# Kernel optimization log

Hardware: AMD Instinct MI355X
Metric: run time of the kernel (lower is better)

Reference implementation:

```python
import jax, jax.numpy as jnp
import numpy as np

N_NODES = 100000
N_EDGES = 3200000
N_GRAPHS = 512
F_IN = 128
HID = 256
N_LABELS = 10


def setup_inputs() -> dict:
    key = jax.random.key(0)
    ks = jax.random.split(key, 16)
    x = jax.random.normal(ks[0], (N_NODES, F_IN), dtype=jnp.float32)
    edge_index = jax.random.randint(ks[1], (2, N_EDGES), 0, N_NODES)
    batch = jnp.sort(jax.random.randint(ks[2], (N_NODES,), 0, N_GRAPHS))
    dims = [(F_IN, HID), (HID, HID), (HID, HID), (HID, HID // 2), (HID // 2, HID // 2), (HID // 2, HID // 4)]
    inp = {"x": x, "edge_index": edge_index, "batch": batch, "primary_idxs_in_batch": 0}
    for i, (di, do) in enumerate(dims, 1):
        inp[f"W{i}"] = jax.random.normal(ks[2 + i], (di, do), dtype=jnp.float32) * (1.0 / np.sqrt(di))
        inp[f"b{i}"] = jnp.zeros((do,), dtype=jnp.float32)
    inp["Wlin"] = jax.random.normal(ks[12], (HID // 4, N_LABELS), dtype=jnp.float32) * (1.0 / np.sqrt(HID // 4))
    inp["blin"] = jnp.zeros((N_LABELS,), dtype=jnp.float32)
    return inp


def _gcn_conv(h, W, b, src, dst, norm):
    # dense transform first (smaller of the two sides), then normalized scatter-aggregate
    m = (h @ W)[src] * norm[:, None]  # [E+N, C_out]
    return jax.ops.segment_sum(m, dst, num_segments=N_NODES) + b


def reference(x, edge_index, batch, primary_idxs_in_batch,
              W1, b1, W2, b2, W3, b3, W4, b4, W5, b5, W6, b6, Wlin, blin):
    loops = jnp.arange(N_NODES, dtype=edge_index.dtype)
    src = jnp.concatenate([edge_index[0], loops])  # A + I (self loops)
    dst = jnp.concatenate([edge_index[1], loops])
    deg = jax.ops.segment_sum(jnp.ones_like(dst, dtype=x.dtype), dst, num_segments=N_NODES)
    dinv = jnp.where(deg > 0, jax.lax.rsqrt(deg), 0.0)
    norm = dinv[src] * dinv[dst]  # D^-1/2 (A+I) D^-1/2 edge weights

    h = jax.nn.relu(_gcn_conv(x, W1, b1, src, dst, norm))
    h = jax.nn.relu(_gcn_conv(h, W2, b2, src, dst, norm))
    h = jax.nn.relu(_gcn_conv(h, W3, b3, src, dst, norm))
    h = jax.nn.relu(_gcn_conv(h, W4, b4, src, dst, norm))
    h = jax.nn.relu(_gcn_conv(h, W5, b5, src, dst, norm))
    h = _gcn_conv(h, W6, b6, src, dst, norm)

    # primary_idxs_in_batch is falsy (0) -> global_mean_pool path
    s = jax.ops.segment_sum(h, batch, num_segments=N_GRAPHS)
    cnt = jax.ops.segment_sum(jnp.ones((N_NODES,), dtype=h.dtype), batch, num_segments=N_GRAPHS)
    pooled = s / jnp.maximum(cnt, 1.0)[:, None]  # [G, HID//4]

    logits = pooled @ Wlin + blin  # [G, labels]
    return (jax.nn.log_softmax(logits, axis=1), jax.nn.softmax(logits, axis=1))
```

## Files before the change

### kernel.cpp

```cpp
#include <hip/hip_runtime.h>
#include <math.h>

#define NN 100000
#define NE 3200000
#define NG 512
#define NBK 782
#define EBLK 782

typedef __attribute__((ext_vector_type(8))) short short8;
typedef __attribute__((ext_vector_type(4))) float f32x4;
typedef __attribute__((ext_vector_type(2))) float f32x2;

__device__ __forceinline__ float bf2f(unsigned short h){
  return __uint_as_float(((unsigned int)h) << 16);
}
__device__ __forceinline__ unsigned short f2bf(float f){
  unsigned int u = __float_as_uint(f);
  unsigned int r = (u + 0x7fffu + ((u >> 16) & 1u)) >> 16;
  return (unsigned short)r;
}
__device__ __forceinline__ void unpack16(uint4 v, float* f){
  f32x2 p;
  p = __builtin_amdgcn_cvt_pk_f32_fp8(v.x, 0); f[0]=p[0];  f[1]=p[1];
  p = __builtin_amdgcn_cvt_pk_f32_fp8(v.x, 1); f[2]=p[0];  f[3]=p[1];
  p = __builtin_amdgcn_cvt_pk_f32_fp8(v.y, 0); f[4]=p[0];  f[5]=p[1];
  p = __builtin_amdgcn_cvt_pk_f32_fp8(v.y, 1); f[6]=p[0];  f[7]=p[1];
  p = __builtin_amdgcn_cvt_pk_f32_fp8(v.z, 0); f[8]=p[0];  f[9]=p[1];
  p = __builtin_amdgcn_cvt_pk_f32_fp8(v.z, 1); f[10]=p[0]; f[11]=p[1];
  p = __builtin_amdgcn_cvt_pk_f32_fp8(v.w, 0); f[12]=p[0]; f[13]=p[1];
  p = __builtin_amdgcn_cvt_pk_f32_fp8(v.w, 1); f[14]=p[0]; f[15]=p[1];
}
__device__ __forceinline__ unsigned char f2fp8(float v){
  int p = __builtin_amdgcn_cvt_pk_fp8_f32(v, v, 0, 0);
  return (unsigned char)p;
}

__global__ __launch_bounds__(256) void hist2_k(const int* __restrict__ ei,
    int* __restrict__ cnt, int* __restrict__ btot){
  __shared__ int lh[NBK];
  int t = threadIdx.x, b = blockIdx.x;
  for (int i=t; i<NBK; i+=256) lh[i] = 0;
  __syncthreads();
  int base = b*4096;
  #pragma unroll
  for (int u=0; u<16; u++){
    int e = base + u*256 + t;
    if (e < NE) atomicAdd(&lh[ei[NE + e] >> 7], 1);
  }
  __syncthreads();
  for (int i=t; i<NBK; i+=256){
    int v = lh[i];
    cnt[b*NBK + i] = v;
    if (v) atomicAdd(&btot[i], v);
  }
}
__global__ void bscan2_k(const int* __restrict__ btot, int* __restrict__ bptr){
  __shared__ int sc[1024];
  int t = threadIdx.x;
  int v = (t < NBK) ? btot[t] : 0;
  sc[t] = v; __syncthreads();
  for (int off=1; off<1024; off<<=1){
    int u = (t>=off) ? sc[t-off] : 0;
    __syncthreads(); sc[t] += u; __syncthreads();
  }
  if (t < NBK) bptr[t] = sc[t] - v;
  if (t == 1023) bptr[NBK] = sc[1023];
}
__global__ __launch_bounds__(256) void bkpfx_k(int* __restrict__ cnt, const int* __restrict__ bptr){
  __shared__ int sc[256];
  int b = blockIdx.x, t = threadIdx.x;
  int carry = bptr[b];
  for (int base=0; base<EBLK; base+=256){
    int blk = base + t;
    int v = (blk < EBLK) ? cnt[blk*NBK + b] : 0;
    sc[t] = v; __syncthreads();
    for (int off=1; off<256; off<<=1){
      int u = (t>=off) ? sc[t-off] : 0;
      __syncthreads(); sc[t] += u; __syncthreads();
    }
    if (blk < EBLK) cnt[blk*NBK + b] = carry + sc[t] - v;
    carry += sc[255];
    __syncthreads();
  }
}
__global__ __launch_bounds__(256) void scat2_k(const int* __restrict__ ei,
    const int* __restrict__ cnt, uint2* __restrict__ ebuf){
  __shared__ int lh[NBK];
  __shared__ int lo[NBK];
  int t = threadIdx.x, b = blockIdx.x;
  for (int i=t; i<NBK; i+=256){ lh[i] = 0; lo[i] = cnt[b*NBK + i]; }
  __syncthreads();
  int base = b*4096;
  #pragma unroll
  for (int u=0; u<16; u++){
    int e = base + u*256 + t;
    if (e < NE){
      int s = ei[e], d = ei[NE + e];
      int bk = d >> 7;
      int r = atomicAdd(&lh[bk], 1);
      ebuf[lo[bk] + r] = make_uint2((unsigned)s, (unsigned)d);
    }
  }
}
__global__ __launch_bounds__(256) void bcsr_k(const uint2* __restrict__ ebuf,
    const int* __restrict__ bptr, int* __restrict__ rp, float* __restrict__ dinv,
    int* __restrict__ col){
  __shared__ int cnt[128];
  __shared__ int off[128];
  __shared__ int sc[128];
  int b = blockIdx.x, t = threadIdx.x;
  int nbase = b << 7;
  int beg = bptr[b], end = bptr[b+1];
  if (t < 128) cnt[t] = 0;
  __syncthreads();
  for (int e = beg + t; e < end; e += 256)
    atomicAdd(&cnt[(int)ebuf[e].y - nbase], 1);
  __syncthreads();
  int v = (t < 128) ? cnt[t] : 0;
  if (t < 128) sc[t] = v;
  __syncthreads();
  for (int o2=1; o2<128; o2<<=1){
    int u = (t < 128 && t >= o2) ? sc[t-o2] : 0;
    __syncthreads();
    if (t < 128) sc[t] += u;
    __syncthreads();
  }
  if (t < 128){
    int node = nbase + t;
    if (node < NN){
      int ex = beg + sc[t] - v;
      rp[node] = ex;
      off[t] = ex;
      dinv[node] = rsqrtf((float)(v + 1));
      cnt[t] = 0;
    }
  }
  if (b == ((NN-1) >> 7) && t == 0) rp[NN] = end;
  __syncthreads();
  for (int e = beg + t; e < end; e += 256){
    uint2 sd = ebuf[e];
    int li = (int)sd.y - nbase;
    int pos = off[li] + atomicAdd(&cnt[li], 1);
    col[pos] = (int)sd.x;
  }
}

__global__ void f2q_k(const float* __restrict__ in, unsigned char* __restrict__ out, int n4){
  int i = blockIdx.x*256 + threadIdx.x;
  if (i < n4){
    float4 v = ((const float4*)in)[i];
    int p = __builtin_amdgcn_cvt_pk_fp8_f32(v.x, v.y, 0, 0);
    p = __builtin_amdgcn_cvt_pk_fp8_f32(v.z, v.w, p, 1);
    ((unsigned int*)out)[i] = (unsigned int)p;
  }
}
__global__ void wswz_all_k(const float* W1, const float* W2, const float* W3,
                           const float* W4, const float* W5, const float* W6,
                           unsigned short* O1, unsigned short* O2, unsigned short* O3,
                           unsigned short* O4, unsigned short* O5, unsigned short* O6){
  int cfg = blockIdx.y;
  int K, N; const float* W; unsigned short* out;
  switch(cfg){
    case 0: K=128; N=256; W=W1; out=O1; break;
    case 1: K=256; N=256; W=W2; out=O2; break;
    case 2: K=256; N=256; W=W3; out=O3; break;
    case 3: K=256; N=128; W=W4; out=O4; break;
    case 4: K=128; N=128; W=W5; out=O5; break;
    default:K=128; N=64;  W=W6; out=O6; break;
  }
  int idx = blockIdx.x*256 + threadIdx.x;
  int total = K*N/8;
  if (idx >= total) return;
  int l = idx & 15;
  int t = idx >> 4; int q = t & 3; t >>= 2;
  int NT = N/16;
  int nt = t % NT, kt = t / NT;
  int kbase = kt*32 + q*8, n = nt*16 + l;
  short8 o;
  #pragma unroll
  for (int j=0;j<8;j++) o[j] = (short)f2bf(W[(size_t)(kbase+j)*N + n]);
  *(short8*)(out + (size_t)idx*8) = o;
}

template<int C, bool SRC_SCALE, bool RELU, bool HAS_BIAS>
__global__ __launch_bounds__(256) void spmm8_k(const unsigned char* __restrict__ in,
    unsigned short* __restrict__ out,
    const int* __restrict__ rp, const int* __restrict__ col,
    const float* __restrict__ dinv, const float* __restrict__ bias)
{
  constexpr int LPR = C/16;
  constexpr int RPW = 64/LPR;
  constexpr int RPB = 4*RPW;
  int tid = threadIdx.x;
  int wv = tid >> 6, lane = tid & 63;
  int sub = lane / LPR, li = lane % LPR;
  int row = blockIdx.x*RPB + wv*RPW + sub;
  if (row >= NN) return;
  int beg = rp[row], end = rp[row+1];
  float di = dinv[row];
  int co = li*16;
  const unsigned char* inb = in + co;
  float acc[16], tmp[16];
  unpack16(*(const uint4*)(inb + (size_t)row*C), acc);
  if (SRC_SCALE){
    #pragma unroll
    for (int v=0;v<16;v++) acc[v] *= di;
  }
  int j = beg;
  for (; j+8 <= end; j += 8){
    int s[8]; uint4 v[8]; float wgt[8];
    #pragma unroll
    for (int u=0;u<8;u++) s[u] = col[j+u];
    #pragma unroll
    for (int u=0;u<8;u++) v[u] = *(const uint4*)(inb + (size_t)s[u]*C);
    if (SRC_SCALE){
      #pragma unroll
      for (int u=0;u<8;u++) wgt[u] = dinv[s[u]];
    }
    #pragma unroll
    for (int u=0;u<8;u++){
      unpack16(v[u], tmp);
      float w = SRC_SCALE ? wgt[u] : 1.f;
      #pragma unroll
      for (int vv=0;vv<16;vv++) acc[vv] = fmaf(w, tmp[vv], acc[vv]);
    }
  }
  for (; j < end; j++){
    int ss = col[j];
    uint4 v = *(const uint4*)(inb + (size_t)ss*C);
    float w = SRC_SCALE ? dinv[ss] : 1.f;
    unpack16(v, tmp);
    #pragma unroll
    for (int vv=0;vv<16;vv++) acc[vv] = fmaf(w, tmp[vv], acc[vv]);
  }
  float bb[16];
  if (HAS_BIAS){
    #pragma unroll
    for (int u=0;u<4;u++) *(float4*)&bb[u*4] = *(const float4*)(bias + co + u*4);
  }
  #pragma unroll
  for (int v=0;v<16;v++){
    acc[v] *= di;
    if (HAS_BIAS) acc[v] += bb[v];
    if (RELU) acc[v] = fmaxf(acc[v], 0.f);
  }
  uint4 o0, o1;
  o0.x = (unsigned int)f2bf(acc[0])  | ((unsigned int)f2bf(acc[1])<<16);
  o0.y = (unsigned int)f2bf(acc[2])  | ((unsigned int)f2bf(acc[3])<<16);
  o0.z = (unsigned int)f2bf(acc[4])  | ((unsigned int)f2bf(acc[5])<<16);
  o0.w = (unsigned int)f2bf(acc[6])  | ((unsigned int)f2bf(acc[7])<<16);
  o1.x = (unsigned int)f2bf(acc[8])  | ((unsigned int)f2bf(acc[9])<<16);
  o1.y = (unsigned int)f2bf(acc[10]) | ((unsigned int)f2bf(acc[11])<<16);
  o1.z = (unsigned int)f2bf(acc[12]) | ((unsigned int)f2bf(acc[13])<<16);
  o1.w = (unsigned int)f2bf(acc[14]) | ((unsigned int)f2bf(acc[15])<<16);
  unsigned short* op = out + (size_t)row*C + co;
  *(uint4*)op = o0;
  *(uint4*)(op + 8) = o1;
}

template<int K, int N, int NB, int EPI>
__global__ __launch_bounds__(256) void mgemm_k(const unsigned short* __restrict__ A,
    const unsigned short* __restrict__ Bsw,
    const float* __restrict__ aux, unsigned short* __restrict__ Cb,
    unsigned char* __restrict__ Cq, int M)
{
  constexpr int NT = NB/16, KT = K/32;
  constexpr int KSTRIDE = (N/16)*64;
  __shared__ short8 Bl[2][NT*64];
  int tid = threadIdx.x;
  int w = tid >> 6, lane = tid & 63;
  int l = lane & 15, q = lane >> 4;
  int nb0 = blockIdx.y * NB;
  int rb = blockIdx.x*256 + w*64;
  const unsigned short* ap[4];
  #pragma unroll
  for (int rt=0; rt<4; rt++){
    int r = min(rb + rt*16 + l, M-1);
    ap[rt] = A + (size_t)r*K + q*8;
  }
  f32x4 acc[4][NT];
  #pragma unroll
  for (int rt=0; rt<4; rt++)
    #pragma unroll
    for (int nt=0; nt<NT; nt++) acc[rt][nt] = (f32x4){0,0,0,0};
  const short8* bsrc = (const short8*)Bsw + (size_t)(nb0/16)*64;
  for (int i=tid; i<NT*64; i+=256) Bl[0][i] = bsrc[i];
  short8 a[4], an[4];
  #pragma unroll
  for (int rt=0; rt<4; rt++) a[rt] = *(const short8*)(ap[rt]);
  for (int kt=0; kt<KT; kt++){
    __syncthreads();
    if (kt+1 < KT){
      const short8* s = bsrc + (size_t)(kt+1)*KSTRIDE;
      for (int i=tid; i<NT*64; i+=256) Bl[(kt+1)&1][i] = s[i];
      #pragma unroll
      for (int rt=0; rt<4; rt++) an[rt] = *(const short8*)(ap[rt] + (kt+1)*32);
    }
    const short8* bl = &Bl[kt&1][0];
    #pragma unroll
    for (int nt=0; nt<NT; nt++){
      short8 bf = bl[nt*64 + q*16 + l];
      acc[0][nt] = __builtin_amdgcn_mfma_f32_16x16x32_bf16(a[0], bf, acc[0][nt], 0,0,0);
      acc[1][nt] = __builtin_amdgcn_mfma_f32_16x16x32_bf16(a[1], bf, acc[1][nt], 0,0,0);
      acc[2][nt] = __builtin_amdgcn_mfma_f32_16x16x32_bf16(a[2], bf, acc[2][nt], 0,0,0);
      acc[3][nt] = __builtin_amdgcn_mfma_f32_16x16x32_bf16(a[3], bf, acc[3][nt], 0,0,0);
    }
    #pragma unroll
    for (int rt=0; rt<4; rt++) a[rt] = an[rt];
  }
  #pragma unroll
  for (int rt=0; rt<4; rt++){
    int rbb = rb + rt*16;
    #pragma unroll
    for (int nt=0; nt<NT; nt++){
      f32x4 av = acc[rt][nt];
      int n = nb0 + nt*16 + l;
      #pragma unroll
      for (int r=0;r<4;r++){
        int row = rbb + q*4 + r;
        if (row < M){
          float v = av[r];
          if (EPI == 0){
            v = fmaxf(v + aux[n], 0.f);
            Cb[(size_t)row*N + n] = f2bf(v);
          } else {
            v *= aux[row];
            Cq[(size_t)row*N + n] = f2fp8(v);
          }
        }
      }
    }
  }
}

__global__ __launch_bounds__(256) void poolhead_k(const unsigned short* __restrict__ h,
    const int* __restrict__ batch, const float* __restrict__ Wlin,
    const float* __restrict__ blin, float* __restrict__ out)
{
  __shared__ int range[2];
  __shared__ float red[4][64];
  __shared__ float pl[64];
  int g = blockIdx.x;
  if (threadIdx.x < 2){
    int target = g + threadIdx.x;
    int lo = 0, hi = NN;
    while (lo < hi){ int m = (lo+hi) >> 1; if (batch[m] < target) lo = m+1; else hi = m; }
    range[threadIdx.x] = lo;
  }
  __syncthreads();
  int lo = range[0], hi = range[1];
  int ch = threadIdx.x & 63, rg = threadIdx.x >> 6;
  float s = 0.f;
  for (int r = lo + rg; r < hi; r += 4) s += bf2f(h[(size_t)r*64 + ch]);
  red[rg][ch] = s; __syncthreads();
  if (rg == 0){
    float tot = red[0][ch] + red[1][ch] + red[2][ch] + red[3][ch];
    pl[ch] = tot / fmaxf((float)(hi - lo), 1.f);
  }
  __syncthreads();
  if (threadIdx.x == 0){
    float l[10];
    #pragma unroll
    for (int j=0;j<10;j++) l[j] = blin[j];
    for (int c=0;c<64;c++){
      float p = pl[c];
      #pragma unroll
      for (int j=0;j<10;j++) l[j] = fmaf(p, Wlin[c*10 + j], l[j]);
    }
    float mx = l[0];
    #pragma unroll
    for (int j=1;j<10;j++) mx = fmaxf(mx, l[j]);
    float e[10]; float se = 0.f;
    #pragma unroll
    for (int j=0;j<10;j++){ e[j] = expf(l[j]-mx); se += e[j]; }
    float lse = logf(se);
    #pragma unroll
    for (int j=0;j<10;j++){
      out[g*10 + j]         = l[j] - mx - lse;
      out[NG*10 + g*10 + j] = e[j] / se;
    }
  }
}

extern "C" void kernel_launch(void* const* d_in, const int* in_sizes, int n_in,
                              void* d_out, int out_size, void* d_ws, size_t ws_size,
                              hipStream_t stream)
{
  const float* x     = (const float*)d_in[0];
  const int*   ei    = (const int*)  d_in[1];
  const int*   batch = (const int*)  d_in[2];
  const float* W1=(const float*)d_in[4],  *b1=(const float*)d_in[5];
  const float* W2=(const float*)d_in[6],  *b2=(const float*)d_in[7];
  const float* W3=(const float*)d_in[8],  *b3=(const float*)d_in[9];
  const float* W4=(const float*)d_in[10], *b4=(const float*)d_in[11];
  const float* W5=(const float*)d_in[12], *b5=(const float*)d_in[13];
  const float* W6=(const float*)d_in[14], *b6=(const float*)d_in[15];
  const float* Wl=(const float*)d_in[16], *bl=(const float*)d_in[17];
  float* out = (float*)d_out;

  char* ws = (char*)d_ws;
  unsigned short* hA  = (unsigned short*)(ws + 0);
  unsigned short* hB  = (unsigned short*)(ws + 51200000);
  unsigned char*  hQ  = (unsigned char*) (ws + 102400000);
  unsigned char*  xq  = (unsigned char*) (ws + 128000000);
  int*   col   = (int*)  (ws + 140800000);
  uint2* ebuf  = (uint2*)(ws + 153600000);
  int*   rp    = (int*)  (ws + 179200000);
  float* dinv  = (float*)(ws + 180000016);
  unsigned short* W1s = (unsigned short*)(ws + 180400016);
  unsigned short* W2s = (unsigned short*)(ws + 180465552);
  unsigned short* W3s = (unsigned short*)(ws + 180596624);
  unsigned short* W4s = (unsigned short*)(ws + 180727696);
  unsigned short* W5s = (unsigned short*)(ws + 180793232);
  unsigned short* W6s = (unsigned short*)(ws + 180826000);
  int*   btot  = (int*)  (ws + 180842896);
  int*   bptr  = (int*)  (ws + 180846032);
  int*   cnt   = (int*)  (ws + 180849184);

  hipMemsetAsync(btot, 0, NBK*4, stream);

  hist2_k <<<EBLK, 256, 0, stream>>>(ei, cnt, btot);
  bscan2_k<<<1, 1024, 0, stream>>>(btot, bptr);
  bkpfx_k <<<NBK, 256, 0, stream>>>(cnt, bptr);
  scat2_k <<<EBLK, 256, 0, stream>>>(ei, cnt, ebuf);
  bcsr_k  <<<NBK, 256, 0, stream>>>(ebuf, bptr, rp, dinv, col);

  wswz_all_k<<<dim3(32,6), 256, 0, stream>>>(W1,W2,W3,W4,W5,W6, W1s,W2s,W3s,W4s,W5s,W6s);
  f2q_k<<<(NN*128/4 + 255)/256, 256, 0, stream>>>(x, xq, NN*128/4);

  const int SQ256 = (NN + 15)/16, SQ128 = (NN + 31)/32, SQ64 = (NN + 63)/64;
  const int GX = (NN + 255)/256;

  spmm8_k<128,true,false,false><<<SQ128,256,0,stream>>>(xq, hA, rp, col, dinv, nullptr);
  mgemm_k<128,256,128,0><<<dim3(GX,2),256,0,stream>>>(hA, W1s, b1, hB, nullptr, NN);
  mgemm_k<256,256,128,1><<<dim3(GX,2),256,0,stream>>>(hB, W2s, dinv, nullptr, hQ, NN);
  spmm8_k<256,false,true,true><<<SQ256,256,0,stream>>>(hQ, hA, rp, col, dinv, b2);
  mgemm_k<256,256,128,1><<<dim3(GX,2),256,0,stream>>>(hA, W3s, dinv, nullptr, hQ, NN);
  spmm8_k<256,false,true,true><<<SQ256,256,0,stream>>>(hQ, hB, rp, col, dinv, b3);
  mgemm_k<256,128,128,1><<<dim3(GX,1),256,0,stream>>>(hB, W4s, dinv, nullptr, hQ, NN);
  spmm8_k<128,false,true,true><<<SQ128,256,0,stream>>>(hQ, hA, rp, col, dinv, b4);
  mgemm_k<128,128,128,1><<<dim3(GX,1),256,0,stream>>>(hA, W5s, dinv, nullptr, hQ, NN);
  spmm8_k<128,false,true,true><<<SQ128,256,0,stream>>>(hQ, hB, rp, col, dinv, b5);
  mgemm_k<128,64,64,1><<<dim3(GX,1),256,0,stream>>>(hB, W6s, dinv, nullptr, hQ, NN);
  spmm8_k<64,false,false,true><<<SQ64,256,0,stream>>>(hQ, hA, rp, col, dinv, b6);

  poolhead_k<<<NG, 256, 0, stream>>>(hA, batch, Wl, bl, out);
}
```

Baseline: 1.187 ms.

## Preload full B column panel into LDS and narrow GEMM N-tile to 64

The GEMM kernel now uses a fixed 64-wide output tile and loads the whole K-by-64 weight slice into shared memory once, before the k loop. This removes the per-k-step double-buffered B loads and the barrier inside the loop. The grid gets twice as many blocks along N, so more parallelism and fewer accumulator registers per thread. In exchange each A row tile is read twice as many times from global memory, and LDS use grows with K.

```diff
diff --git a/kernel.cpp b/kernel.cpp
--- a/kernel.cpp
+++ b/kernel.cpp
@@ -258,20 +258,29 @@
   *(uint4*)(op + 8) = o1;
 }
 
-template<int K, int N, int NB, int EPI>
+template<int K, int N, int EPI>
 __global__ __launch_bounds__(256) void mgemm_k(const unsigned short* __restrict__ A,
     const unsigned short* __restrict__ Bsw,
     const float* __restrict__ aux, unsigned short* __restrict__ Cb,
     unsigned char* __restrict__ Cq, int M)
 {
-  constexpr int NT = NB/16, KT = K/32;
-  constexpr int KSTRIDE = (N/16)*64;
-  __shared__ short8 Bl[2][NT*64];
+  constexpr int NT = 4;
+  constexpr int KT = K/32;
+  constexpr int NTF = N/16;
+  __shared__ short8 Bl[KT*NT*64];
   int tid = threadIdx.x;
   int w = tid >> 6, lane = tid & 63;
   int l = lane & 15, q = lane >> 4;
-  int nb0 = blockIdx.y * NB;
+  int nb0 = blockIdx.y * 64;
   int rb = blockIdx.x*256 + w*64;
+  {
+    const short8* bsrc = (const short8*)Bsw;
+    for (int i = tid; i < KT*NT*64; i += 256){
+      int kt = i >> 8;
+      int rem = i & 255;
+      Bl[i] = bsrc[(kt*NTF + (nb0 >> 4))*64 + rem];
+    }
+  }
   const unsigned short* ap[4];
   #pragma unroll
   for (int rt=0; rt<4; rt++){
@@ -283,20 +292,16 @@
   for (int rt=0; rt<4; rt++)
     #pragma unroll
     for (int nt=0; nt<NT; nt++) acc[rt][nt] = (f32x4){0,0,0,0};
-  const short8* bsrc = (const short8*)Bsw + (size_t)(nb0/16)*64;
-  for (int i=tid; i<NT*64; i+=256) Bl[0][i] = bsrc[i];
   short8 a[4], an[4];
   #pragma unroll
   for (int rt=0; rt<4; rt++) a[rt] = *(const short8*)(ap[rt]);
+  __syncthreads();
   for (int kt=0; kt<KT; kt++){
-    __syncthreads();
     if (kt+1 < KT){
-      const short8* s = bsrc + (size_t)(kt+1)*KSTRIDE;
-      for (int i=tid; i<NT*64; i+=256) Bl[(kt+1)&1][i] = s[i];
       #pragma unroll
       for (int rt=0; rt<4; rt++) an[rt] = *(const short8*)(ap[rt] + (kt+1)*32);
     }
-    const short8* bl = &Bl[kt&1][0];
+    const short8* bl = &Bl[kt << 8];
     #pragma unroll
     for (int nt=0; nt<NT; nt++){
       short8 bf = bl[nt*64 + q*16 + l];
@@ -432,16 +437,16 @@
   const int GX = (NN + 255)/256;
 
   spmm8_k<128,true,false,false><<<SQ128,256,0,stream>>>(xq, hA, rp, col, dinv, nullptr);
-  mgemm_k<128,256,128,0><<<dim3(GX,2),256,0,stream>>>(hA, W1s, b1, hB, nullptr, NN);
-  mgemm_k<256,256,128,1><<<dim3(GX,2),256,0,stream>>>(hB, W2s, dinv, nullptr, hQ, NN);
+  mgemm_k<128,256,0><<<dim3(GX,4),256,0,stream>>>(hA, W1s, b1, hB, nullptr, NN);
+  mgemm_k<256,256,1><<<dim3(GX,4),256,0,stream>>>(hB, W2s, dinv, nullptr, hQ, NN);
   spmm8_k<256,false,true,true><<<SQ256,256,0,stream>>>(hQ, hA, rp, col, dinv, b2);
-  mgemm_k<256,256,128,1><<<dim3(GX,2),256,0,stream>>>(hA, W3s, dinv, nullptr, hQ, NN);
+  mgemm_k<256,256,1><<<dim3(GX,4),256,0,stream>>>(hA, W3s, dinv, nullptr, hQ, NN);
   spmm8_k<256,false,true,true><<<SQ256,256,0,stream>>>(hQ, hB, rp, col, dinv, b3);
-  mgemm_k<256,128,128,1><<<dim3(GX,1),256,0,stream>>>(hB, W4s, dinv, nullptr, hQ, NN);
+  mgemm_k<256,128,1><<<dim3(GX,2),256,0,stream>>>(hB, W4s, dinv, nullptr, hQ, NN);
   spmm8_k<128,false,true,true><<<SQ128,256,0,stream>>>(hQ, hA, rp, col, dinv, b4);
-  mgemm_k<128,128,128,1><<<dim3(GX,1),256,0,stream>>>(hA, W5s, dinv, nullptr, hQ, NN);
+  mgemm_k<128,128,1><<<dim3(GX,2),256,0,stream>>>(hA, W5s, dinv, nullptr, hQ, NN);
   spmm8_k<128,false,true,true><<<SQ128,256,0,stream>>>(hQ, hB, rp, col, dinv, b5);
-  mgemm_k<128,64,64,1><<<dim3(GX,1),256,0,stream>>>(hB, W6s, dinv, nullptr, hQ, NN);
+  mgemm_k<128,64,1><<<dim3(GX,1),256,0,stream>>>(hB, W6s, dinv, nullptr, hQ, NN);
   spmm8_k<64,false,false,true><<<SQ64,256,0,stream>>>(hQ, hA, rp, col, dinv, b6);
 
   poolhead_k<<<NG, 256, 0, stream>>>(hA, batch, Wl, bl, out);
```

Result: faster. 1.104 ms (-7.0%).
